# Kernel tuning notes

Hardware: AMD Instinct MI355X
Metric: run time of the kernel (lower is better)

## Reference

```python
import jax, jax.numpy as jnp
import numpy as np

KS = 3          # deform kernel size
N = KS * KS     # sampling points per output pixel
PAD = 1         # zero padding

def conv2d(x, w, stride, padding):
    return jax.lax.conv_general_dilated(
        x, w, (stride, stride), [(padding, padding), (padding, padding)],
        dimension_numbers=('NCHW', 'OIHW', 'NCHW'))

def _gather(x_flat, qx, qy, Wp):
    # x_flat: [b, c, Hp*Wp]; qx, qy: [b, h, w, N] int32 -> [b, c, h, w, N]
    b = qx.shape[0]; c = x_flat.shape[1]
    idx = (qx * Wp + qy).reshape(b, 1, -1)
    out = jnp.take_along_axis(x_flat, jnp.broadcast_to(idx, (b, c, idx.shape[-1])), axis=2)
    return out.reshape(b, c, qx.shape[1], qx.shape[2], qx.shape[3])

def deform_conv(x, w_off, b_off, w_conv):
    # learned per-pixel offsets: [b, 2N, h, w] (first N = x-offsets, last N = y-offsets)
    offset = conv2d(x, w_off, 1, PAD) + b_off[None, :, None, None]
    b, _, h, w = offset.shape
    x_pad = jnp.pad(x, ((0, 0), (0, 0), (PAD, PAD), (PAD, PAD)))
    Hp, Wp = x_pad.shape[2], x_pad.shape[3]
    # kernel-relative offsets p_n in {-1,0,1}^2
    pn_x, pn_y = jnp.meshgrid(jnp.arange(-(KS // 2), KS // 2 + 1),
                              jnp.arange(-(KS // 2), KS // 2 + 1), indexing='ij')
    p_n = jnp.concatenate([pn_x.reshape(-1), pn_y.reshape(-1)]).reshape(1, 2 * N, 1, 1)
    # base grid p_0 (1..h, 1..w in padded coordinates)
    p0_x, p0_y = jnp.meshgrid(jnp.arange(1, h + 1), jnp.arange(1, w + 1), indexing='ij')
    p_0 = jnp.concatenate([jnp.tile(p0_x[None], (N, 1, 1)),
                           jnp.tile(p0_y[None], (N, 1, 1))])[None]  # [1, 2N, h, w]
    p = (p_0 + p_n).astype(offset.dtype) + offset                   # [b, 2N, h, w]
    p = jnp.transpose(p, (0, 2, 3, 1))                              # [b, h, w, 2N]
    px, py = p[..., :N], p[..., N:]
    q = jnp.floor(jax.lax.stop_gradient(p))
    qlt_x = jnp.clip(q[..., :N], 0, Hp - 1); qlt_y = jnp.clip(q[..., N:], 0, Wp - 1)
    qrb_x = jnp.clip(q[..., :N] + 1, 0, Hp - 1); qrb_y = jnp.clip(q[..., N:] + 1, 0, Wp - 1)
    px = jnp.clip(px, 0, Hp - 1); py = jnp.clip(py, 0, Wp - 1)
    # bilinear weights (classic DCN formulation)
    g_lt = (1 + (qlt_x - px)) * (1 + (qlt_y - py))
    g_rb = (1 - (qrb_x - px)) * (1 - (qrb_y - py))
    g_lb = (1 + (qlt_x - px)) * (1 - (qrb_y - py))
    g_rt = (1 - (qrb_x - px)) * (1 + (qlt_y - py))
    x_flat = x_pad.reshape(b, x_pad.shape[1], -1)
    qi = lambda a: a.astype(jnp.int32)
    x_lt = _gather(x_flat, qi(qlt_x), qi(qlt_y), Wp)
    x_rb = _gather(x_flat, qi(qrb_x), qi(qrb_y), Wp)
    x_lb = _gather(x_flat, qi(qlt_x), qi(qrb_y), Wp)
    x_rt = _gather(x_flat, qi(qrb_x), qi(qlt_y), Wp)
    xo = (g_lt[:, None] * x_lt + g_rb[:, None] * x_rb
          + g_lb[:, None] * x_lb + g_rt[:, None] * x_rt)  # [b, c, h, w, N]
    c = xo.shape[1]
    # unfold N -> (ks, ks) blocks: [b, c, h*ks, w*ks]
    xo = xo.reshape(b, c, h, w, KS, KS).transpose(0, 1, 2, 4, 3, 5).reshape(b, c, h * KS, w * KS)
    return conv2d(xo, w_conv, KS, 0)  # stride=ks aggregation, no bias

def reference(x, w_off, b_off, w_conv, w_fc, b_fc):
    y = jax.nn.relu(deform_conv(x, w_off, b_off, w_conv))          # [b, 8, 28, 28]
    y = jax.lax.reduce_window(y, -jnp.inf, jax.lax.max,
                              (1, 1, 2, 2), (1, 1, 2, 2), 'VALID')  # [b, 8, 14, 14]
    y = y.reshape(y.shape[0], -1)
    return y @ w_fc.T + b_fc

def setup_inputs() -> dict:
    key = jax.random.key(0)
    k1, k2, k3, k4 = jax.random.split(key, 4)
    B = 4096
    return {
        'x': jax.random.normal(k1, (B, 1, 28, 28), dtype=jnp.float32),
        'w_off': jax.random.normal(k2, (18, 1, 3, 3), dtype=jnp.float32) * 0.1,
        'b_off': jnp.zeros((18,), dtype=jnp.float32),
        'w_conv': jax.random.normal(k3, (8, 1, 3, 3), dtype=jnp.float32) * 0.3,
        'w_fc': jax.random.normal(k4, (10, 8 * 14 * 14), dtype=jnp.float32) * 0.02,
        'b_fc': jnp.zeros((10,), dtype=jnp.float32),
    }
```

## Files before the change

kernel.cpp:

```cpp
#include <hip/hip_runtime.h>


#define HH 28
#define WW 28
#define WP 30
#define NPOS 784
#define NPOOL 1568
#define CELLS 196

__global__ __launch_bounds__(256) void deform_net_kernel(
    const float* __restrict__ x,
    const float* __restrict__ w_off,
    const float* __restrict__ b_off,
    const float* __restrict__ w_conv,
    const float* __restrict__ w_fc,
    const float* __restrict__ b_fc,
    float* __restrict__ out)
{
    __shared__ float xs[900];
    __shared__ float wo_s[162];
    __shared__ float bo_s[18];
    __shared__ float wc_s[72];
    __shared__ float red[4][10];

    const int b   = blockIdx.x;
    const int tid = threadIdx.x;

    if (tid < 162) wo_s[tid] = w_off[tid];
    if (tid < 18)  bo_s[tid] = b_off[tid];
    if (tid < 72)  wc_s[tid] = w_conv[tid];

    const float* xb = x + (size_t)b * NPOS;
    for (int i = tid; i < 900; i += 256) {
        int r = i / WP, c = i % WP;
        float v = 0.f;
        if (r >= 1 && r <= HH && c >= 1 && c <= WW)
            v = xb[(r - 1) * WW + (c - 1)];
        xs[i] = v;
    }
    __syncthreads();

    float fc[10];
    #pragma unroll
    for (int c = 0; c < 10; c++) fc[c] = 0.f;

    if (tid < CELLS) {
        const int ph = tid / 14, pw = tid % 14;
        const int h0 = 2 * ph, w0 = 2 * pw;

        float nb[16];
        #pragma unroll
        for (int i = 0; i < 4; i++)
            #pragma unroll
            for (int j = 0; j < 4; j++)
                nb[i * 4 + j] = xs[(h0 + i) * WP + (w0 + j)];

        float acc[4][8];
        #pragma unroll
        for (int p = 0; p < 4; p++)
            #pragma unroll
            for (int o = 0; o < 8; o++) acc[p][o] = 0.f;

        #pragma unroll
        for (int k = 0; k < 9; k++) {
            const int kx = k / 3, ky = k % 3;
            #pragma unroll
            for (int p = 0; p < 4; p++) {
                const int dh = p >> 1, dw = p & 1;

                float offx = bo_s[k], offy = bo_s[k + 9];
                #pragma unroll
                for (int t = 0; t < 9; t++) {
                    float nv = nb[(dh + t / 3) * 4 + (dw + t % 3)];
                    offx = fmaf(wo_s[k * 9 + t],       nv, offx);
                    offy = fmaf(wo_s[(k + 9) * 9 + t], nv, offy);
                }

                float p_x = (float)(h0 + dh + kx) + offx;
                float p_y = (float)(w0 + dw + ky) + offy;

                float q0x = floorf(p_x), q0y = floorf(p_y);
                float qltx = __builtin_amdgcn_fmed3f(q0x,       0.f, 29.f);
                float qlty = __builtin_amdgcn_fmed3f(q0y,       0.f, 29.f);
                float qrbx = __builtin_amdgcn_fmed3f(q0x + 1.f, 0.f, 29.f);
                float qrby = __builtin_amdgcn_fmed3f(q0y + 1.f, 0.f, 29.f);
                float px   = __builtin_amdgcn_fmed3f(p_x,       0.f, 29.f);
                float py   = __builtin_amdgcn_fmed3f(p_y,       0.f, 29.f);

                float gltx = 1.f + (qltx - px);
                float glty = 1.f + (qlty - py);
                float grbx = 1.f - (qrbx - px);
                float grby = 1.f - (qrby - py);

                int ilx = (int)qltx, ily = (int)qlty;
                int irx = (int)qrbx, iry = (int)qrby;

                float xlt = xs[ilx * WP + ily];
                float xrb = xs[irx * WP + iry];
                float xlb = xs[ilx * WP + iry];
                float xrt = xs[irx * WP + ily];

                float s = gltx * (glty * xlt + grby * xlb)
                        + grbx * (glty * xrt + grby * xrb);

                #pragma unroll
                for (int o = 0; o < 8; o++)
                    acc[p][o] = fmaf(wc_s[o * 9 + k], s, acc[p][o]);
            }
        }

        #pragma unroll
        for (int o = 0; o < 8; o++) {
            float m = fmaxf(fmaxf(acc[0][o], acc[1][o]),
                            fmaxf(acc[2][o], acc[3][o]));
            m = fmaxf(m, 0.f);
            const float* wrow = w_fc + o * CELLS + tid;
            #pragma unroll
            for (int c = 0; c < 10; c++)
                fc[c] = fmaf(m, wrow[c * NPOOL], fc[c]);
        }
    }

    #pragma unroll
    for (int c = 0; c < 10; c++) {
        #pragma unroll
        for (int sh = 32; sh > 0; sh >>= 1)
            fc[c] += __shfl_down(fc[c], sh, 64);
    }
    const int wave = tid >> 6, lane = tid & 63;
    if (lane == 0) {
        #pragma unroll
        for (int c = 0; c < 10; c++) red[wave][c] = fc[c];
    }
    __syncthreads();
    if (tid < 10)
        out[b * 10 + tid] = red[0][tid] + red[1][tid] + red[2][tid]
                          + red[3][tid] + b_fc[tid];
}

extern "C" void kernel_launch(void* const* d_in, const int* in_sizes, int n_in,
                              void* d_out, int out_size, void* d_ws, size_t ws_size,
                              hipStream_t stream) {
    const float* x      = (const float*)d_in[0];
    const float* w_off  = (const float*)d_in[1];
    const float* b_off  = (const float*)d_in[2];
    const float* w_conv = (const float*)d_in[3];
    const float* w_fc   = (const float*)d_in[4];
    const float* b_fc   = (const float*)d_in[5];
    float* out = (float*)d_out;

    const int B = in_sizes[0] / NPOS;
    deform_net_kernel<<<B, 256, 0, stream>>>(x, w_off, b_off, w_conv, w_fc, b_fc, out);
}
```

Before: 126.2 us.

## Pack pooled cells across images into full blocks with atomic output accumulation

The kernel previously ran one block per image, so 60 of 256 threads sat idle. It now flattens all images' 196 pooled cells into a global index, so each 256-thread block spans up to three images. The images' padded tiles are staged in LDS with a row pitch of 31 to cut bank conflicts. Wave partial sums are split per image slot and combined with atomicAdd into an output zeroed by a memset. This adds a memset launch, atomics, more LDS staging and extra address arithmetic, and it makes the float summation order nondeterministic.

```diff
diff --git a/kernel.cpp b/kernel.cpp
--- a/kernel.cpp
+++ b/kernel.cpp
@@ -3,10 +3,12 @@
 
 #define HH 28
 #define WW 28
-#define WP 30
+#define WPL 31
+#define IMG_LDS 930
 #define NPOS 784
 #define NPOOL 1568
 #define CELLS 196
+#define TPB 256
 
 __global__ __launch_bounds__(256) void deform_net_kernel(
     const float* __restrict__ x,
@@ -15,37 +17,48 @@
     const float* __restrict__ w_conv,
     const float* __restrict__ w_fc,
     const float* __restrict__ b_fc,
-    float* __restrict__ out)
+    float* __restrict__ out,
+    int Btot)
 {
-    __shared__ float xs[900];
+    __shared__ float xs[3 * IMG_LDS];
     __shared__ float wo_s[162];
     __shared__ float bo_s[18];
     __shared__ float wc_s[72];
-    __shared__ float red[4][10];
-
-    const int b   = blockIdx.x;
-    const int tid = threadIdx.x;
+    __shared__ float red[4][3][10];
+
+    const int tid   = threadIdx.x;
+    const int cell0 = blockIdx.x * TPB;
+    const int imgFirst = cell0 / CELLS;
+    const int total = Btot * CELLS;
 
     if (tid < 162) wo_s[tid] = w_off[tid];
     if (tid < 18)  bo_s[tid] = b_off[tid];
     if (tid < 72)  wc_s[tid] = w_conv[tid];
-
-    const float* xb = x + (size_t)b * NPOS;
-    for (int i = tid; i < 900; i += 256) {
-        int r = i / WP, c = i % WP;
-        float v = 0.f;
-        if (r >= 1 && r <= HH && c >= 1 && c <= WW)
-            v = xb[(r - 1) * WW + (c - 1)];
-        xs[i] = v;
+    if (tid < 120) (&red[0][0][0])[tid] = 0.f;
+
+    for (int i = tid; i < 3 * 900; i += TPB) {
+        int s = i / 900, v = i - s * 900;
+        int img = imgFirst + s;
+        int r = v / 30, c = v - r * 30;
+        float val = 0.f;
+        if (img < Btot && r >= 1 && r <= HH && c >= 1 && c <= WW)
+            val = x[(size_t)img * NPOS + (r - 1) * WW + (c - 1)];
+        xs[s * IMG_LDS + r * WPL + c] = val;
     }
     __syncthreads();
+
+    const int cell = cell0 + tid;
+    const int img  = cell / CELLS;
+    const int cim  = cell - img * CELLS;
+    const int slot = img - imgFirst;
+    const float* xsl = xs + slot * IMG_LDS;
 
     float fc[10];
     #pragma unroll
     for (int c = 0; c < 10; c++) fc[c] = 0.f;
 
-    if (tid < CELLS) {
-        const int ph = tid / 14, pw = tid % 14;
+    if (cell < total) {
+        const int ph = cim / 14, pw = cim - (cim / 14) * 14;
         const int h0 = 2 * ph, w0 = 2 * pw;
 
         float nb[16];
@@ -53,7 +66,7 @@
         for (int i = 0; i < 4; i++)
             #pragma unroll
             for (int j = 0; j < 4; j++)
-                nb[i * 4 + j] = xs[(h0 + i) * WP + (w0 + j)];
+                nb[i * 4 + j] = xsl[(h0 + i) * WPL + (w0 + j)];
 
         float acc[4][8];
         #pragma unroll
@@ -95,10 +108,10 @@
                 int ilx = (int)qltx, ily = (int)qlty;
                 int irx = (int)qrbx, iry = (int)qrby;
 
-                float xlt = xs[ilx * WP + ily];
-                float xrb = xs[irx * WP + iry];
-                float xlb = xs[ilx * WP + iry];
-                float xrt = xs[irx * WP + ily];
+                float xlt = xsl[ilx * WPL + ily];
+                float xrb = xsl[irx * WPL + iry];
+                float xlb = xsl[ilx * WPL + iry];
+                float xrt = xsl[irx * WPL + ily];
 
                 float s = gltx * (glty * xlt + grby * xlb)
                         + grbx * (glty * xrt + grby * xrb);
@@ -114,28 +127,64 @@
             float m = fmaxf(fmaxf(acc[0][o], acc[1][o]),
                             fmaxf(acc[2][o], acc[3][o]));
             m = fmaxf(m, 0.f);
-            const float* wrow = w_fc + o * CELLS + tid;
+            const float* wrow = w_fc + o * CELLS + cim;
             #pragma unroll
             for (int c = 0; c < 10; c++)
                 fc[c] = fmaf(m, wrow[c * NPOOL], fc[c]);
         }
     }
 
-    #pragma unroll
-    for (int c = 0; c < 10; c++) {
-        #pragma unroll
-        for (int sh = 32; sh > 0; sh >>= 1)
-            fc[c] += __shfl_down(fc[c], sh, 64);
-    }
     const int wave = tid >> 6, lane = tid & 63;
-    if (lane == 0) {
-        #pragma unroll
-        for (int c = 0; c < 10; c++) red[wave][c] = fc[c];
+    const int wc0 = cell0 + (wave << 6);
+    const int sLo = wc0 / CELLS - imgFirst;
+    const int sHi = (wc0 + 63) / CELLS - imgFirst;
+
+    if (sLo == sHi) {
+        #pragma unroll
+        for (int c = 0; c < 10; c++)
+            #pragma unroll
+            for (int sh = 32; sh > 0; sh >>= 1)
+                fc[c] += __shfl_down(fc[c], sh, 64);
+        if (lane == 0) {
+            #pragma unroll
+            for (int c = 0; c < 10; c++) red[wave][sLo][c] = fc[c];
+        }
+    } else {
+        float va[10];
+        const bool lo = (slot == sLo);
+        #pragma unroll
+        for (int c = 0; c < 10; c++) {
+            va[c] = lo ? fc[c] : 0.f;
+            fc[c] = lo ? 0.f : fc[c];
+        }
+        #pragma unroll
+        for (int c = 0; c < 10; c++)
+            #pragma unroll
+            for (int sh = 32; sh > 0; sh >>= 1) {
+                va[c] += __shfl_down(va[c], sh, 64);
+                fc[c] += __shfl_down(fc[c], sh, 64);
+            }
+        if (lane == 0) {
+            #pragma unroll
+            for (int c = 0; c < 10; c++) {
+                red[wave][sLo][c] = va[c];
+                red[wave][sHi][c] = fc[c];
+            }
+        }
     }
     __syncthreads();
-    if (tid < 10)
-        out[b * 10 + tid] = red[0][tid] + red[1][tid] + red[2][tid]
-                          + red[3][tid] + b_fc[tid];
+
+    if (tid < 30) {
+        const int s = tid / 10, c = tid - (tid / 10) * 10;
+        const int oimg = imgFirst + s;
+        if (oimg < Btot) {
+            float v = red[0][s][c] + red[1][s][c]
+                    + red[2][s][c] + red[3][s][c];
+            const int c0im = oimg * CELLS - cell0;
+            if (c0im >= 0 && c0im < TPB) v += b_fc[c];
+            if (v != 0.f) atomicAdd(out + oimg * 10 + c, v);
+        }
+    }
 }
 
 extern "C" void kernel_launch(void* const* d_in, const int* in_sizes, int n_in,
@@ -150,5 +199,8 @@
     float* out = (float*)d_out;
 
     const int B = in_sizes[0] / NPOS;
-    deform_net_kernel<<<B, 256, 0, stream>>>(x, w_off, b_off, w_conv, w_fc, b_fc, out);
+    hipMemsetAsync(d_out, 0, (size_t)B * 10 * sizeof(float), stream);
+    const int nblk = (B * CELLS + TPB - 1) / TPB;
+    deform_net_kernel<<<nblk, TPB, 0, stream>>>(x, w_off, b_off, w_conv,
+                                                w_fc, b_fc, out, B);
 }
```

Measured after the change: 139.8 us. 1.11x slower.

## Process four images per block with interleaved threads to fill idle lanes

Applied to the files above, without the earlier changes.

Each block now handles four images instead of one. Threads are interleaved by image slot (tid&3), and each thread loops over up to four pooled cells. Before, 60 of 256 threads sat idle and each block amortized its weight loads over a single image. The reduction changes to xor-shuffles that keep the per-image partial sums separate. The cost is four times more LDS per block and a serial loop per thread, which could lower occupancy or add latency.

```diff
diff --git a/kernel.cpp b/kernel.cpp
--- a/kernel.cpp
+++ b/kernel.cpp
@@ -1,12 +1,12 @@
 #include <hip/hip_runtime.h>
 
 
-#define HH 28
-#define WW 28
-#define WP 30
-#define NPOS 784
+#define NPOS  784
 #define NPOOL 1568
 #define CELLS 196
+#define TPB   256
+#define WP    30
+#define PIMG  900
 
 __global__ __launch_bounds__(256) void deform_net_kernel(
     const float* __restrict__ x,
@@ -15,127 +15,144 @@
     const float* __restrict__ w_conv,
     const float* __restrict__ w_fc,
     const float* __restrict__ b_fc,
-    float* __restrict__ out)
+    float* __restrict__ out,
+    int Btot)
 {
-    __shared__ float xs[900];
+    __shared__ float xs[4 * PIMG];
     __shared__ float wo_s[162];
     __shared__ float bo_s[18];
     __shared__ float wc_s[72];
-    __shared__ float red[4][10];
+    __shared__ float red[4][4][10];
 
-    const int b   = blockIdx.x;
-    const int tid = threadIdx.x;
+    const int tid      = threadIdx.x;
+    const int imgFirst = blockIdx.x * 4;
 
     if (tid < 162) wo_s[tid] = w_off[tid];
     if (tid < 18)  bo_s[tid] = b_off[tid];
     if (tid < 72)  wc_s[tid] = w_conv[tid];
 
-    const float* xb = x + (size_t)b * NPOS;
-    for (int i = tid; i < 900; i += 256) {
-        int r = i / WP, c = i % WP;
-        float v = 0.f;
-        if (r >= 1 && r <= HH && c >= 1 && c <= WW)
-            v = xb[(r - 1) * WW + (c - 1)];
-        xs[i] = v;
+    for (int i = tid; i < 4 * PIMG; i += TPB) {
+        int s = i / PIMG;
+        int v = i - s * PIMG;
+        int r = v / WP, c = v - r * WP;
+        int img = imgFirst + s;
+        float val = 0.f;
+        if (img < Btot && r >= 1 && r <= 28 && c >= 1 && c <= 28)
+            val = x[(size_t)img * NPOS + (r - 1) * 28 + (c - 1)];
+        xs[i] = val;
     }
     __syncthreads();
+
+    const int imgSlot = tid & 3;
+    const int lc      = tid >> 2;
+    const float* __restrict__ xsl = xs + imgSlot * PIMG;
 
     float fc[10];
     #pragma unroll
     for (int c = 0; c < 10; c++) fc[c] = 0.f;
 
-    if (tid < CELLS) {
-        const int ph = tid / 14, pw = tid % 14;
-        const int h0 = 2 * ph, w0 = 2 * pw;
+    #pragma unroll 1
+    for (int it = 0; it < 4; ++it) {
+        const int cell = lc + (it << 6);
+        if (cell < CELLS) {
+            const int ph = cell / 14, pw = cell - (cell / 14) * 14;
+            const int h0 = 2 * ph, w0 = 2 * pw;
 
-        float nb[16];
-        #pragma unroll
-        for (int i = 0; i < 4; i++)
+            float nb[16];
             #pragma unroll
-            for (int j = 0; j < 4; j++)
-                nb[i * 4 + j] = xs[(h0 + i) * WP + (w0 + j)];
+            for (int i = 0; i < 4; i++)
+                #pragma unroll
+                for (int j = 0; j < 4; j++)
+                    nb[i * 4 + j] = xsl[(h0 + i) * WP + (w0 + j)];
 
-        float acc[4][8];
-        #pragma unroll
-        for (int p = 0; p < 4; p++)
+            float acc[4][8];
             #pragma unroll
-            for (int o = 0; o < 8; o++) acc[p][o] = 0.f;
+            for (int p = 0; p < 4; p++)
+                #pragma unroll
+                for (int o = 0; o < 8; o++) acc[p][o] = 0.f;
 
-        #pragma unroll
-        for (int k = 0; k < 9; k++) {
-            const int kx = k / 3, ky = k % 3;
             #pragma unroll
-            for (int p = 0; p < 4; p++) {
-                const int dh = p >> 1, dw = p & 1;
+            for (int k = 0; k < 9; k++) {
+                const int kx = k / 3, ky = k % 3;
+                #pragma unroll
+                for (int p = 0; p < 4; p++) {
+                    const int dh = p >> 1, dw = p & 1;
 
-                float offx = bo_s[k], offy = bo_s[k + 9];
+                    float offx = bo_s[k], offy = bo_s[k + 9];
+                    #pragma unroll
+                    for (int t = 0; t < 9; t++) {
+                        float nv = nb[(dh + t / 3) * 4 + (dw + t % 3)];
+                        offx = fmaf(wo_s[k * 9 + t],       nv, offx);
+                        offy = fmaf(wo_s[(k + 9) * 9 + t], nv, offy);
+                    }
+
+                    float p_x = (float)(h0 + dh + kx) + offx;
+                    float p_y = (float)(w0 + dw + ky) + offy;
+
+                    float q0x = floorf(p_x), q0y = floorf(p_y);
+                    float qltx = __builtin_amdgcn_fmed3f(q0x,       0.f, 29.f);
+                    float qlty = __builtin_amdgcn_fmed3f(q0y,       0.f, 29.f);
+                    float qrbx = __builtin_amdgcn_fmed3f(q0x + 1.f, 0.f, 29.f);
+                    float qrby = __builtin_amdgcn_fmed3f(q0y + 1.f, 0.f, 29.f);
+                    float px   = __builtin_amdgcn_fmed3f(p_x,       0.f, 29.f);
+                    float py   = __builtin_amdgcn_fmed3f(p_y,       0.f, 29.f);
+
+                    float gltx = 1.f + (qltx - px);
+                    float glty = 1.f + (qlty - py);
+                    float grbx = 1.f - (qrbx - px);
+                    float grby = 1.f - (qrby - py);
+
+                    int ilx = (int)qltx, ily = (int)qlty;
+                    int irx = (int)qrbx, iry = (int)qrby;
+
+                    float xlt = xsl[ilx * WP + ily];
+                    float xrb = xsl[irx * WP + iry];
+                    float xlb = xsl[ilx * WP + iry];
+                    float xrt = xsl[irx * WP + ily];
+
+                    float s = gltx * (glty * xlt + grby * xlb)
+                            + grbx * (glty * xrt + grby * xrb);
+
+                    #pragma unroll
+                    for (int o = 0; o < 8; o++)
+                        acc[p][o] = fmaf(wc_s[o * 9 + k], s, acc[p][o]);
+                }
+            }
+
+            #pragma unroll
+            for (int o = 0; o < 8; o++) {
+                float m = fmaxf(fmaxf(acc[0][o], acc[1][o]),
+                                fmaxf(acc[2][o], acc[3][o]));
+                m = fmaxf(m, 0.f);
+                const float* wrow = w_fc + o * CELLS + cell;
                 #pragma unroll
-                for (int t = 0; t < 9; t++) {
-                    float nv = nb[(dh + t / 3) * 4 + (dw + t % 3)];
-                    offx = fmaf(wo_s[k * 9 + t],       nv, offx);
-                    offy = fmaf(wo_s[(k + 9) * 9 + t], nv, offy);
-                }
-
-                float p_x = (float)(h0 + dh + kx) + offx;
-                float p_y = (float)(w0 + dw + ky) + offy;
-
-                float q0x = floorf(p_x), q0y = floorf(p_y);
-                float qltx = __builtin_amdgcn_fmed3f(q0x,       0.f, 29.f);
-                float qlty = __builtin_amdgcn_fmed3f(q0y,       0.f, 29.f);
-                float qrbx = __builtin_amdgcn_fmed3f(q0x + 1.f, 0.f, 29.f);
-                float qrby = __builtin_amdgcn_fmed3f(q0y + 1.f, 0.f, 29.f);
-                float px   = __builtin_amdgcn_fmed3f(p_x,       0.f, 29.f);
-                float py   = __builtin_amdgcn_fmed3f(p_y,       0.f, 29.f);
-
-                float gltx = 1.f + (qltx - px);
-                float glty = 1.f + (qlty - py);
-                float grbx = 1.f - (qrbx - px);
-                float grby = 1.f - (qrby - py);
-
-                int ilx = (int)qltx, ily = (int)qlty;
-                int irx = (int)qrbx, iry = (int)qrby;
-
-                float xlt = xs[ilx * WP + ily];
-                float xrb = xs[irx * WP + iry];
-                float xlb = xs[ilx * WP + iry];
-                float xrt = xs[irx * WP + ily];
-
-                float s = gltx * (glty * xlt + grby * xlb)
-                        + grbx * (glty * xrt + grby * xrb);
-
-                #pragma unroll
-                for (int o = 0; o < 8; o++)
-                    acc[p][o] = fmaf(wc_s[o * 9 + k], s, acc[p][o]);
+                for (int c = 0; c < 10; c++)
+                    fc[c] = fmaf(m, wrow[c * NPOOL], fc[c]);
             }
-        }
-
-        #pragma unroll
-        for (int o = 0; o < 8; o++) {
-            float m = fmaxf(fmaxf(acc[0][o], acc[1][o]),
-                            fmaxf(acc[2][o], acc[3][o]));
-            m = fmaxf(m, 0.f);
-            const float* wrow = w_fc + o * CELLS + tid;
-            #pragma unroll
-            for (int c = 0; c < 10; c++)
-                fc[c] = fmaf(m, wrow[c * NPOOL], fc[c]);
         }
     }
 
     #pragma unroll
     for (int c = 0; c < 10; c++) {
-        #pragma unroll
-        for (int sh = 32; sh > 0; sh >>= 1)
-            fc[c] += __shfl_down(fc[c], sh, 64);
+        fc[c] += __shfl_xor(fc[c], 4, 64);
+        fc[c] += __shfl_xor(fc[c], 8, 64);
+        fc[c] += __shfl_xor(fc[c], 16, 64);
+        fc[c] += __shfl_xor(fc[c], 32, 64);
     }
     const int wave = tid >> 6, lane = tid & 63;
-    if (lane == 0) {
+    if (lane < 4) {
         #pragma unroll
-        for (int c = 0; c < 10; c++) red[wave][c] = fc[c];
+        for (int c = 0; c < 10; c++) red[wave][lane][c] = fc[c];
     }
     __syncthreads();
-    if (tid < 10)
-        out[b * 10 + tid] = red[0][tid] + red[1][tid] + red[2][tid]
-                          + red[3][tid] + b_fc[tid];
+
+    if (tid < 40) {
+        const int s = tid / 10, c = tid - (tid / 10) * 10;
+        const int img = imgFirst + s;
+        if (img < Btot)
+            out[img * 10 + c] = red[0][s][c] + red[1][s][c]
+                              + red[2][s][c] + red[3][s][c] + b_fc[c];
+    }
 }
 
 extern "C" void kernel_launch(void* const* d_in, const int* in_sizes, int n_in,
@@ -150,5 +167,7 @@
     float* out = (float*)d_out;
 
     const int B = in_sizes[0] / NPOS;
-    deform_net_kernel<<<B, 256, 0, stream>>>(x, w_off, b_off, w_conv, w_fc, b_fc, out);
+    const int nblk = (B + 3) / 4;
+    deform_net_kernel<<<nblk, TPB, 0, stream>>>(x, w_off, b_off, w_conv,
+                                                w_fc, b_fc, out, B);
 }
```

New measurement: 189.3 us. +49.9%, slower.

## Assign one thread per output pixel and split FC outputs across quad lanes

Applied to the files above, without the earlier changes.

The block grows from 256 to 832 threads so each thread computes one of the 784 deform-conv output pixels, not a 2x2 pooling cell. The 2x2 max-pool is done with xor shuffles inside each quad of lanes. The FC layer is split so each lane in a quad handles two or three of the ten output classes, which cuts per-thread register use and the shuffle-reduction work. This trades the old per-thread reuse of the 4x4 neighbourhood for more parallelism and less serial work per thread, at the cost of larger blocks and some duplicated neighbourhood loads.

```diff
diff --git a/kernel.cpp b/kernel.cpp
--- a/kernel.cpp
+++ b/kernel.cpp
@@ -1,14 +1,14 @@
 #include <hip/hip_runtime.h>
 
 
-#define HH 28
-#define WW 28
-#define WP 30
-#define NPOS 784
+#define NPOS  784
 #define NPOOL 1568
 #define CELLS 196
+#define TPB   832
+#define WP    30
+#define PIMG  900
 
-__global__ __launch_bounds__(256) void deform_net_kernel(
+__global__ __launch_bounds__(832) void deform_net_kernel(
     const float* __restrict__ x,
     const float* __restrict__ w_off,
     const float* __restrict__ b_off,
@@ -17,125 +17,154 @@
     const float* __restrict__ b_fc,
     float* __restrict__ out)
 {
-    __shared__ float xs[900];
+    __shared__ float xs[PIMG];
     __shared__ float wo_s[162];
     __shared__ float bo_s[18];
     __shared__ float wc_s[72];
-    __shared__ float red[4][10];
+    __shared__ float red[13][4][3];
 
+    const int tid = threadIdx.x;
     const int b   = blockIdx.x;
-    const int tid = threadIdx.x;
 
     if (tid < 162) wo_s[tid] = w_off[tid];
     if (tid < 18)  bo_s[tid] = b_off[tid];
     if (tid < 72)  wc_s[tid] = w_conv[tid];
 
-    const float* xb = x + (size_t)b * NPOS;
-    for (int i = tid; i < 900; i += 256) {
-        int r = i / WP, c = i % WP;
+    const float* __restrict__ xb = x + (size_t)b * NPOS;
+    for (int i = tid; i < PIMG; i += TPB) {
+        int r = i / WP, c = i - r * WP;
         float v = 0.f;
-        if (r >= 1 && r <= HH && c >= 1 && c <= WW)
-            v = xb[(r - 1) * WW + (c - 1)];
+        if (r >= 1 && r <= 28 && c >= 1 && c <= 28)
+            v = xb[(r - 1) * 28 + (c - 1)];
         xs[i] = v;
     }
     __syncthreads();
 
-    float fc[10];
+    const int cell = tid >> 2;
+    const int p    = tid & 3;
+
+    float m[8];
     #pragma unroll
-    for (int c = 0; c < 10; c++) fc[c] = 0.f;
+    for (int o = 0; o < 8; o++) m[o] = 0.f;
+    float fc0 = 0.f, fc1 = 0.f, fc2 = 0.f;
 
-    if (tid < CELLS) {
-        const int ph = tid / 14, pw = tid % 14;
-        const int h0 = 2 * ph, w0 = 2 * pw;
+    if (tid < NPOS) {
+        const int ph = cell / 14, pw = cell - (cell / 14) * 14;
+        const int h = 2 * ph + (p >> 1);
+        const int w = 2 * pw + (p & 1);
 
-        float nb[16];
+        float nb[9];
         #pragma unroll
-        for (int i = 0; i < 4; i++)
+        for (int i = 0; i < 3; i++)
             #pragma unroll
-            for (int j = 0; j < 4; j++)
-                nb[i * 4 + j] = xs[(h0 + i) * WP + (w0 + j)];
+            for (int j = 0; j < 3; j++)
+                nb[i * 3 + j] = xs[(h + i) * WP + (w + j)];
 
-        float acc[4][8];
+        float acc[8];
         #pragma unroll
-        for (int p = 0; p < 4; p++)
-            #pragma unroll
-            for (int o = 0; o < 8; o++) acc[p][o] = 0.f;
+        for (int o = 0; o < 8; o++) acc[o] = 0.f;
 
         #pragma unroll
         for (int k = 0; k < 9; k++) {
             const int kx = k / 3, ky = k % 3;
+
+            float offx = bo_s[k], offy = bo_s[k + 9];
             #pragma unroll
-            for (int p = 0; p < 4; p++) {
-                const int dh = p >> 1, dw = p & 1;
+            for (int t = 0; t < 9; t++) {
+                float nv = nb[t];
+                offx = fmaf(wo_s[k * 9 + t],       nv, offx);
+                offy = fmaf(wo_s[(k + 9) * 9 + t], nv, offy);
+            }
 
-                float offx = bo_s[k], offy = bo_s[k + 9];
-                #pragma unroll
-                for (int t = 0; t < 9; t++) {
-                    float nv = nb[(dh + t / 3) * 4 + (dw + t % 3)];
-                    offx = fmaf(wo_s[k * 9 + t],       nv, offx);
-                    offy = fmaf(wo_s[(k + 9) * 9 + t], nv, offy);
-                }
+            float p_x = (float)(h + kx) + offx;
+            float p_y = (float)(w + ky) + offy;
 
-                float p_x = (float)(h0 + dh + kx) + offx;
-                float p_y = (float)(w0 + dw + ky) + offy;
+            float q0x = floorf(p_x), q0y = floorf(p_y);
+            float qltx = __builtin_amdgcn_fmed3f(q0x,       0.f, 29.f);
+            float qlty = __builtin_amdgcn_fmed3f(q0y,       0.f, 29.f);
+            float qrbx = __builtin_amdgcn_fmed3f(q0x + 1.f, 0.f, 29.f);
+            float qrby = __builtin_amdgcn_fmed3f(q0y + 1.f, 0.f, 29.f);
+            float px   = __builtin_amdgcn_fmed3f(p_x,       0.f, 29.f);
+            float py   = __builtin_amdgcn_fmed3f(p_y,       0.f, 29.f);
 
-                float q0x = floorf(p_x), q0y = floorf(p_y);
-                float qltx = __builtin_amdgcn_fmed3f(q0x,       0.f, 29.f);
-                float qlty = __builtin_amdgcn_fmed3f(q0y,       0.f, 29.f);
-                float qrbx = __builtin_amdgcn_fmed3f(q0x + 1.f, 0.f, 29.f);
-                float qrby = __builtin_amdgcn_fmed3f(q0y + 1.f, 0.f, 29.f);
-                float px   = __builtin_amdgcn_fmed3f(p_x,       0.f, 29.f);
-                float py   = __builtin_amdgcn_fmed3f(p_y,       0.f, 29.f);
+            float gltx = 1.f + (qltx - px);
+            float glty = 1.f + (qlty - py);
+            float grbx = 1.f - (qrbx - px);
+            float grby = 1.f - (qrby - py);
 
-                float gltx = 1.f + (qltx - px);
-                float glty = 1.f + (qlty - py);
-                float grbx = 1.f - (qrbx - px);
-                float grby = 1.f - (qrby - py);
+            int ilx = (int)qltx, ily = (int)qlty;
+            int irx = (int)qrbx, iry = (int)qrby;
 
-                int ilx = (int)qltx, ily = (int)qlty;
-                int irx = (int)qrbx, iry = (int)qrby;
+            float xlt = xs[ilx * WP + ily];
+            float xrb = xs[irx * WP + iry];
+            float xlb = xs[ilx * WP + iry];
+            float xrt = xs[irx * WP + ily];
 
-                float xlt = xs[ilx * WP + ily];
-                float xrb = xs[irx * WP + iry];
-                float xlb = xs[ilx * WP + iry];
-                float xrt = xs[irx * WP + ily];
+            float s = gltx * (glty * xlt + grby * xlb)
+                    + grbx * (glty * xrt + grby * xrb);
 
-                float s = gltx * (glty * xlt + grby * xlb)
-                        + grbx * (glty * xrt + grby * xrb);
-
-                #pragma unroll
-                for (int o = 0; o < 8; o++)
-                    acc[p][o] = fmaf(wc_s[o * 9 + k], s, acc[p][o]);
-            }
+            #pragma unroll
+            for (int o = 0; o < 8; o++)
+                acc[o] = fmaf(wc_s[o * 9 + k], s, acc[o]);
         }
 
         #pragma unroll
-        for (int o = 0; o < 8; o++) {
-            float m = fmaxf(fmaxf(acc[0][o], acc[1][o]),
-                            fmaxf(acc[2][o], acc[3][o]));
-            m = fmaxf(m, 0.f);
-            const float* wrow = w_fc + o * CELLS + tid;
+        for (int o = 0; o < 8; o++) m[o] = acc[o];
+    }
+
+    #pragma unroll
+    for (int o = 0; o < 8; o++) {
+        m[o] = fmaxf(m[o], __shfl_xor(m[o], 1, 64));
+        m[o] = fmaxf(m[o], __shfl_xor(m[o], 2, 64));
+        m[o] = fmaxf(m[o], 0.f);
+    }
+
+    if (tid < NPOS) {
+        const int l3 = tid & 3;
+        {
+            const float* wcol = w_fc + l3 * NPOOL + cell;
+            float s0 = 0.f;
             #pragma unroll
-            for (int c = 0; c < 10; c++)
-                fc[c] = fmaf(m, wrow[c * NPOOL], fc[c]);
+            for (int o = 0; o < 8; o++) s0 = fmaf(m[o], wcol[o * CELLS], s0);
+            fc0 = s0;
+        }
+        {
+            const float* wcol = w_fc + (l3 + 4) * NPOOL + cell;
+            float s0 = 0.f;
+            #pragma unroll
+            for (int o = 0; o < 8; o++) s0 = fmaf(m[o], wcol[o * CELLS], s0);
+            fc1 = s0;
+        }
+        if (l3 < 2) {
+            const float* wcol = w_fc + (l3 + 8) * NPOOL + cell;
+            float s0 = 0.f;
+            #pragma unroll
+            for (int o = 0; o < 8; o++) s0 = fmaf(m[o], wcol[o * CELLS], s0);
+            fc2 = s0;
         }
     }
 
     #pragma unroll
-    for (int c = 0; c < 10; c++) {
-        #pragma unroll
-        for (int sh = 32; sh > 0; sh >>= 1)
-            fc[c] += __shfl_down(fc[c], sh, 64);
+    for (int sh = 4; sh <= 32; sh <<= 1) {
+        fc0 += __shfl_xor(fc0, sh, 64);
+        fc1 += __shfl_xor(fc1, sh, 64);
+        fc2 += __shfl_xor(fc2, sh, 64);
     }
     const int wave = tid >> 6, lane = tid & 63;
-    if (lane == 0) {
-        #pragma unroll
-        for (int c = 0; c < 10; c++) red[wave][c] = fc[c];
+    if (lane < 4) {
+        red[wave][lane][0] = fc0;
+        red[wave][lane][1] = fc1;
+        red[wave][lane][2] = fc2;
     }
     __syncthreads();
-    if (tid < 10)
-        out[b * 10 + tid] = red[0][tid] + red[1][tid] + red[2][tid]
-                          + red[3][tid] + b_fc[tid];
+
+    if (tid < 10) {
+        const int r4 = tid & 3, j = tid >> 2;
+        float v = b_fc[tid];
+        #pragma unroll
+        for (int wv = 0; wv < 13; wv++) v += red[wv][r4][j];
+        out[b * 10 + tid] = v;
+    }
 }
 
 extern "C" void kernel_launch(void* const* d_in, const int* in_sizes, int n_in,
@@ -150,5 +179,6 @@
     float* out = (float*)d_out;
 
     const int B = in_sizes[0] / NPOS;
-    deform_net_kernel<<<B, 256, 0, stream>>>(x, w_off, b_off, w_conv, w_fc, b_fc, out);
+    deform_net_kernel<<<B, TPB, 0, stream>>>(x, w_off, b_off, w_conv,
+                                             w_fc, b_fc, out);
 }
```

Result: slower. 180.6 us (+43.0%).
